# Kernel tuning notes

Hardware: AMD Instinct MI355X
Metric: run time of the kernel (lower is better)

## Reference

```python
import jax, jax.numpy as jnp
import numpy as np

NMUL = 1
NEARZERO = 1e-5
ROUTING_LEN = 15
N_DYN = 3
N_STATIC = 13  # layout includes parRT, parAC (present in STATIC_PARAM_NAMES but unused in the step)


def _descale(x, lb, ub):
    return lb + x * (ub - lb)


def setup_inputs() -> dict:
    key = jax.random.key(0)
    k1, k2, k3 = jax.random.split(key, 3)
    T, G = 365, 50000
    u = jax.random.uniform(k1, (T, G, 3), dtype=jnp.float32)
    prcp = u[..., 0] * 10.0                 # mm/day
    tmean = (u[..., 1] - 0.3) * 20.0        # degC, roughly [-6, 14] so snow branch is exercised
    pet = u[..., 2] * 5.0                   # mm/day
    forcing = jnp.stack([prcp, tmean, pet], axis=-1)
    dyn_raw = jax.random.uniform(k2, (T, G, N_DYN * NMUL), dtype=jnp.float32)
    static_raw = jax.random.uniform(k3, (G, N_STATIC * NMUL + 2), dtype=jnp.float32)
    return {"forcing": forcing, "dyn_raw": dyn_raw, "static_raw": static_raw}


def _hbv_forward(forcing, dyn_raw, static_raw):
    T, G, _ = forcing.shape
    dt = forcing.dtype
    # --- descale dynamic params (per-timestep): parBETA, parK0, parBETAET ---
    dyn = dyn_raw.reshape(T, G, N_DYN, NMUL)
    parBETA = _descale(dyn[:, :, 0], 1.0, 6.0)
    parK0 = _descale(dyn[:, :, 1], 0.05, 0.9)
    parBETAET = _descale(dyn[:, :, 2], 0.3, 5.0)
    # --- descale static params ---
    st = static_raw[:, :N_STATIC * NMUL].reshape(G, N_STATIC, NMUL)
    parFC = _descale(st[:, 0], 50.0, 1000.0)
    parK1 = _descale(st[:, 1], 0.01, 0.5)
    parK2 = _descale(st[:, 2], 0.001, 0.2)
    parLP = _descale(st[:, 3], 0.2, 1.0)
    parPERC = _descale(st[:, 4], 0.0, 10.0)
    parUZL = _descale(st[:, 5], 0.0, 100.0)
    parTT = _descale(st[:, 6], -2.5, 2.5)
    parCFMAX = _descale(st[:, 7], 0.5, 10.0)
    parCFR = _descale(st[:, 8], 0.0, 0.1)
    parCWH = _descale(st[:, 9], 0.0, 0.2)
    parC = _descale(st[:, 10], 0.0, 1.0)
    rout = static_raw[:, N_STATIC * NMUL:]
    rout_a = _descale(rout[:, 0], 0.0, 2.9)
    rout_b = _descale(rout[:, 1], 0.0, 6.5)

    Pm = jnp.broadcast_to(forcing[..., 0:1], (T, G, NMUL))
    Tm = jnp.broadcast_to(forcing[..., 1:2], (T, G, NMUL))
    PETm = jnp.broadcast_to(forcing[..., 2:3], (T, G, NMUL))

    def step(carry, xs):
        SNOWPACK, MELTWATER, SM, SUZ, SLZ = carry
        PRECIP, TEMP, PET, pBETA, pK0, pBETAET = xs
        is_rain = (TEMP >= parTT).astype(dt)
        RAIN = PRECIP * is_rain
        SNOW = PRECIP * (1.0 - is_rain)
        SNOWPACK = SNOWPACK + SNOW
        melt = jnp.minimum(jnp.maximum(parCFMAX * (TEMP - parTT), 0.0), SNOWPACK)
        MELTWATER = MELTWATER + melt
        SNOWPACK = SNOWPACK - melt
        refreezing = jnp.minimum(jnp.maximum(parCFR * parCFMAX * (parTT - TEMP), 0.0), MELTWATER)
        SNOWPACK = SNOWPACK + refreezing
        MELTWATER = MELTWATER - refreezing
        tosoil = jnp.maximum(MELTWATER - parCWH * SNOWPACK, 0.0)
        MELTWATER = MELTWATER - tosoil
        soil_wetness = jnp.clip((SM / parFC) ** pBETA, 0.0, 1.0)
        recharge = (RAIN + tosoil) * soil_wetness
        SM = SM + RAIN + tosoil - recharge
        excess = jnp.maximum(SM - parFC, 0.0)
        SM = SM - excess
        evapfactor = jnp.clip((SM / (parLP * parFC)) ** pBETAET, 0.0, 1.0)
        ETact = jnp.minimum(SM, PET * evapfactor)
        SM = jnp.maximum(SM - ETact, NEARZERO)
        capillary = jnp.minimum(SLZ, parC * SLZ * (1.0 - jnp.minimum(SM / parFC, 1.0)))
        SM = jnp.maximum(SM + capillary, NEARZERO)
        SLZ = jnp.maximum(SLZ - capillary, NEARZERO)
        SUZ = SUZ + recharge + excess
        PERC = jnp.minimum(SUZ, parPERC)
        SUZ = SUZ - PERC
        Q0 = pK0 * jnp.maximum(SUZ - parUZL, 0.0)
        SUZ = SUZ - Q0
        Q1 = parK1 * SUZ
        SUZ = SUZ - Q1
        SLZ = jnp.maximum(SLZ + PERC, 0.0)
        Q2 = parK2 * SLZ
        SLZ = SLZ - Q2
        return (SNOWPACK, MELTWATER, SM, SUZ, SLZ), Q0 + Q1 + Q2

    init = tuple(jnp.full((G, NMUL), 0.001, dtype=dt) for _ in range(5))
    _, Qall = jax.lax.scan(step, init, (Pm, Tm, PETm, parBETA, parK0, parBETAET))
    Qsim = Qall.mean(axis=-1)  # [T, G]: average over nmul components

    # --- gamma unit-hydrograph routing (hydroDL UH_gamma + causal conv, lenF = 15) ---
    aa = jax.nn.relu(rout_a) + 0.1      # shape param, [G]
    theta = jax.nn.relu(rout_b) + 0.5   # scale param, [G]
    t = jnp.arange(0.5, ROUTING_LEN, dtype=dt)[:, None]  # [15, 1] midpoints
    w = (t ** (aa - 1.0)) * jnp.exp(-t / theta) / (jnp.exp(jax.lax.lgamma(aa)) * theta ** aa)
    w = w / w.sum(axis=0)  # [15, G], normalized UH weights
    Qpad = jnp.pad(Qsim, ((ROUTING_LEN - 1, 0), (0, 0)))
    # causal conv: Qrout[t] = sum_k w[k] * Qsim[t-k]; fixed 15-tap loop
    Qrout = sum(w[k] * jax.lax.dynamic_slice_in_dim(Qpad, ROUTING_LEN - 1 - k, T, axis=0)
                for k in range(ROUTING_LEN))
    return Qrout  # streamflow [T, G]


def reference(forcing, dyn_raw, static_raw):
    return _hbv_forward(forcing, dyn_raw, static_raw)
```

## Files before the change

### kernel.cpp

```cpp
#include <hip/hip_runtime.h>

#define NEARZERO 1e-5f
#define RLEN 15
#define LOG2E 1.4426950408889634f

typedef float f32x4 __attribute__((ext_vector_type(4)));
struct __attribute__((packed, aligned(4))) uld4 { f32x4 v; };

static __device__ __forceinline__ f32x4 ld4u(const float* p) {
    return ((const uld4*)p)->v;
}

struct Par { float FC, invFC, invLPFC, K1, K2, PERC, UZL, TT, CFMAX, CFRC, CWH, C; };

#define SB() __builtin_amdgcn_sched_barrier(0)

template<int PH>
__device__ __forceinline__ float one_step(
    float P, float TEMP, float PET, float dx, float dy, float dz,
    const Par& pr,
    float& SNOWPACK, float& MELTWATER, float& SM, float& SUZ, float& SLZ,
    float (&acc)[RLEN], const float (&w)[RLEN])
{
    const float pBETA   = fmaf(dx, 5.0f, 1.0f);
    const float pK0     = fmaf(dy, 0.85f, 0.05f);
    const float pBETAET = fmaf(dz, 4.7f, 0.3f);

    const float d    = TEMP - pr.TT;
    const float RAIN = (d >= 0.0f) ? P : 0.0f;
    const float SNOW = P - RAIN;
    SNOWPACK += SNOW;
    const float melt = __builtin_amdgcn_fmed3f(pr.CFMAX * d, 0.0f, SNOWPACK);
    MELTWATER += melt;
    SNOWPACK  -= melt;
    const float refr = __builtin_amdgcn_fmed3f(pr.CFRC * (0.0f - d), 0.0f, MELTWATER);
    SNOWPACK  += refr;
    MELTWATER -= refr;
    const float tosoil = fmaxf(fmaf(-pr.CWH, SNOWPACK, MELTWATER), 0.0f);
    MELTWATER -= tosoil;

    const float sw = fminf(exp2f(pBETA * __log2f(SM * pr.invFC)), 1.0f);
    const float rt = RAIN + tosoil;
    const float recharge = rt * sw;
    SM = SM + rt - recharge;
    const float excess = fmaxf(SM - pr.FC, 0.0f);
    SM -= excess;
    const float ef = fminf(exp2f(pBETAET * __log2f(SM * pr.invLPFC)), 1.0f);
    const float ETact = fminf(SM, PET * ef);
    SM = fmaxf(SM - ETact, NEARZERO);
    const float capillary = pr.C * SLZ * (1.0f - fminf(SM * pr.invFC, 1.0f));
    SM  = fmaxf(SM + capillary, NEARZERO);
    SLZ = fmaxf(SLZ - capillary, NEARZERO);

    SUZ += recharge + excess;
    const float PERC = fminf(SUZ, pr.PERC);
    SUZ -= PERC;
    const float Q0 = pK0 * fmaxf(SUZ - pr.UZL, 0.0f);
    SUZ -= Q0;
    const float Q1 = pr.K1 * SUZ;
    SUZ -= Q1;
    SLZ += PERC;
    const float Q2 = pr.K2 * SLZ;
    SLZ -= Q2;
    const float Qsim = Q0 + Q1 + Q2;

    const float qr = fmaf(w[0], Qsim, acc[PH]);
    acc[PH] = 0.0f;
#pragma unroll
    for (int k = 1; k < RLEN; ++k) {
        const int j = (PH + k) % RLEN;
        acc[j] = fmaf(w[k], Qsim, acc[j]);
    }
    return qr;
}

template<int PH0>
__device__ __forceinline__ void comp5(
    const f32x4 (&F)[5], const f32x4 (&D)[5], const Par& pr,
    float& SP_, float& MW, float& SM, float& SUZ, float& SLZ,
    float (&acc)[RLEN], const float (&w)[RLEN],
    float*& outp, int G, bool guard)
{
    float qr;
    qr = one_step<(PH0 + 0) % RLEN>(F[0].x, F[0].y, F[0].z, D[0].x, D[0].y, D[0].z,
                                    pr, SP_, MW, SM, SUZ, SLZ, acc, w);
    if (guard) __builtin_nontemporal_store(qr, outp);
    outp += G;
    qr = one_step<(PH0 + 1) % RLEN>(F[1].x, F[1].y, F[1].z, D[1].x, D[1].y, D[1].z,
                                    pr, SP_, MW, SM, SUZ, SLZ, acc, w);
    if (guard) __builtin_nontemporal_store(qr, outp);
    outp += G;
    qr = one_step<(PH0 + 2) % RLEN>(F[2].x, F[2].y, F[2].z, D[2].x, D[2].y, D[2].z,
                                    pr, SP_, MW, SM, SUZ, SLZ, acc, w);
    if (guard) __builtin_nontemporal_store(qr, outp);
    outp += G;
    qr = one_step<(PH0 + 3) % RLEN>(F[3].x, F[3].y, F[3].z, D[3].x, D[3].y, D[3].z,
                                    pr, SP_, MW, SM, SUZ, SLZ, acc, w);
    if (guard) __builtin_nontemporal_store(qr, outp);
    outp += G;
    qr = one_step<(PH0 + 4) % RLEN>(F[4].x, F[4].y, F[4].z, D[4].x, D[4].y, D[4].z,
                                    pr, SP_, MW, SM, SUZ, SLZ, acc, w);
    if (guard) __builtin_nontemporal_store(qr, outp);
    outp += G;
}

__global__ __launch_bounds__(64, 1) void hbv_kernel(
    const float* __restrict__ forcing,
    const float* __restrict__ dynr,
    const float* __restrict__ statr,
    float* __restrict__ out,
    int G)
{
    const int lane = threadIdx.x;
    const int g  = blockIdx.x * 64 + lane;
    const int gc = (g < G) ? g : (G - 1);
    const bool guard = (g < G);

    const float* sp = statr + (size_t)gc * 15;
    Par pr;
    pr.FC    = fmaf(sp[0], 950.0f, 50.0f);
    pr.K1    = fmaf(sp[1], 0.49f, 0.01f);
    pr.K2    = fmaf(sp[2], 0.199f, 0.001f);
    const float parLP = fmaf(sp[3], 0.8f, 0.2f);
    pr.PERC  = sp[4] * 10.0f;
    pr.UZL   = sp[5] * 100.0f;
    pr.TT    = fmaf(sp[6], 5.0f, -2.5f);
    pr.CFMAX = fmaf(sp[7], 9.5f, 0.5f);
    pr.CFRC  = (sp[8] * 0.1f) * pr.CFMAX;
    pr.CWH   = sp[9] * 0.2f;
    pr.C     = sp[10];
    const float rout_a = sp[13] * 2.9f;
    const float rout_b = sp[14] * 6.5f;
    pr.invFC   = 1.0f / pr.FC;
    pr.invLPFC = 1.0f / (parLP * pr.FC);

    const float aa    = fmaxf(rout_a, 0.0f) + 0.1f;
    const float theta = fmaxf(rout_b, 0.0f) + 0.5f;
    const float am1   = aa - 1.0f;
    const float nitl2 = -LOG2E / theta;
    float w[RLEN];
    float wsum = 0.0f;
#pragma unroll
    for (int k = 0; k < RLEN; ++k) {
        const float tk = (float)k + 0.5f;
        w[k] = exp2f(am1 * __log2f(tk) + tk * nitl2);
        wsum += w[k];
    }
    const float winv = 1.0f / wsum;
#pragma unroll
    for (int k = 0; k < RLEN; ++k) w[k] *= winv;

    float SP_ = 0.001f, MW = 0.001f, SM = 0.001f, SUZ = 0.001f, SLZ = 0.001f;
    float acc[RLEN];
#pragma unroll
    for (int k = 0; k < RLEN; ++k) acc[k] = 0.0f;

    const size_t sT = (size_t)G * 3;
    const float* pF = forcing + (size_t)gc * 3;
    const float* pD = dynr    + (size_t)gc * 3;
    float* outp = out + g;

    f32x4 AF[5], AD[5], BF[5], BD[5], CF[5], CD[5];

#define LOADG(BFv, BDv, tb) do { \
    const float* fp_ = pF + (size_t)(tb) * sT; \
    const float* dp_ = pD + (size_t)(tb) * sT; \
    BFv[0] = ld4u(fp_); BDv[0] = ld4u(dp_); fp_ += sT; dp_ += sT; \
    BFv[1] = ld4u(fp_); BDv[1] = ld4u(dp_); fp_ += sT; dp_ += sT; \
    BFv[2] = ld4u(fp_); BDv[2] = ld4u(dp_); fp_ += sT; dp_ += sT; \
    BFv[3] = ld4u(fp_); BDv[3] = ld4u(dp_); fp_ += sT; dp_ += sT; \
    BFv[4] = ld4u(fp_); BDv[4] = ld4u(dp_); \
} while (0)

    LOADG(AF, AD, 0);
    LOADG(BF, BD, 5);

    for (int i = 0; i < 23; ++i) {
        const int tb = i * 15;
        SB(); LOADG(CF, CD, tb + 10); SB();
        comp5<0>(AF, AD, pr, SP_, MW, SM, SUZ, SLZ, acc, w, outp, G, guard);
        SB(); LOADG(AF, AD, tb + 15); SB();
        comp5<5>(BF, BD, pr, SP_, MW, SM, SUZ, SLZ, acc, w, outp, G, guard);
        SB(); LOADG(BF, BD, tb + 20); SB();
        comp5<10>(CF, CD, pr, SP_, MW, SM, SUZ, SLZ, acc, w, outp, G, guard);
    }
    SB(); LOADG(CF, CD, 355); SB();
    comp5<0>(AF, AD, pr, SP_, MW, SM, SUZ, SLZ, acc, w, outp, G, guard);
    SB(); LOADG(AF, AD, 360); SB();
    comp5<5>(BF, BD, pr, SP_, MW, SM, SUZ, SLZ, acc, w, outp, G, guard);
    comp5<10>(CF, CD, pr, SP_, MW, SM, SUZ, SLZ, acc, w, outp, G, guard);
    comp5<0>(AF, AD, pr, SP_, MW, SM, SUZ, SLZ, acc, w, outp, G, guard);
#undef LOADG
}

extern "C" void kernel_launch(void* const* d_in, const int* in_sizes, int n_in,
                              void* d_out, int out_size, void* d_ws, size_t ws_size,
                              hipStream_t stream) {
    const float* forcing = (const float*)d_in[0];
    const float* dynr    = (const float*)d_in[1];
    const float* statr   = (const float*)d_in[2];
    float* out = (float*)d_out;

    const int G = in_sizes[2] / 15;
    const int block = 64;
    const int grid  = (G + block - 1) / block;
    hbv_kernel<<<grid, block, 0, stream>>>(forcing, dynr, statr, out, G);
}
```

Measured before the change: 120.8 us.

## Replace batched register prefetch with per-step loads staged through an LDS ring

Drops the three-buffer, five-step batch prefetch of 16-byte unaligned vector loads. Each timestep now issues 12-byte loads for a row eight steps ahead into a five-slot register set, then moves an earlier register set into a 15-row shared-memory ring that the compute step reads from. The aim is a deeper, evenly spread prefetch pipeline with less register pressure and no over-read past the end of the row. In exchange every step adds LDS writes and reads, and a sched_barrier sits on each step.

```diff
diff --git a/kernel.cpp b/kernel.cpp
--- a/kernel.cpp
+++ b/kernel.cpp
@@ -4,16 +4,13 @@
 #define RLEN 15
 #define LOG2E 1.4426950408889634f
 
-typedef float f32x4 __attribute__((ext_vector_type(4)));
-struct __attribute__((packed, aligned(4))) uld4 { f32x4 v; };
-
-static __device__ __forceinline__ f32x4 ld4u(const float* p) {
-    return ((const uld4*)p)->v;
+struct __attribute__((packed, aligned(4))) F3 { float x, y, z; };
+
+static __device__ __forceinline__ F3 ld3f(const float* p) {
+    return *reinterpret_cast<const F3*>(p);
 }
 
 struct Par { float FC, invFC, invLPFC, K1, K2, PERC, UZL, TT, CFMAX, CFRC, CWH, C; };
-
-#define SB() __builtin_amdgcn_sched_barrier(0)
 
 template<int PH>
 __device__ __forceinline__ float one_step(
@@ -74,36 +71,6 @@
     return qr;
 }
 
-template<int PH0>
-__device__ __forceinline__ void comp5(
-    const f32x4 (&F)[5], const f32x4 (&D)[5], const Par& pr,
-    float& SP_, float& MW, float& SM, float& SUZ, float& SLZ,
-    float (&acc)[RLEN], const float (&w)[RLEN],
-    float*& outp, int G, bool guard)
-{
-    float qr;
-    qr = one_step<(PH0 + 0) % RLEN>(F[0].x, F[0].y, F[0].z, D[0].x, D[0].y, D[0].z,
-                                    pr, SP_, MW, SM, SUZ, SLZ, acc, w);
-    if (guard) __builtin_nontemporal_store(qr, outp);
-    outp += G;
-    qr = one_step<(PH0 + 1) % RLEN>(F[1].x, F[1].y, F[1].z, D[1].x, D[1].y, D[1].z,
-                                    pr, SP_, MW, SM, SUZ, SLZ, acc, w);
-    if (guard) __builtin_nontemporal_store(qr, outp);
-    outp += G;
-    qr = one_step<(PH0 + 2) % RLEN>(F[2].x, F[2].y, F[2].z, D[2].x, D[2].y, D[2].z,
-                                    pr, SP_, MW, SM, SUZ, SLZ, acc, w);
-    if (guard) __builtin_nontemporal_store(qr, outp);
-    outp += G;
-    qr = one_step<(PH0 + 3) % RLEN>(F[3].x, F[3].y, F[3].z, D[3].x, D[3].y, D[3].z,
-                                    pr, SP_, MW, SM, SUZ, SLZ, acc, w);
-    if (guard) __builtin_nontemporal_store(qr, outp);
-    outp += G;
-    qr = one_step<(PH0 + 4) % RLEN>(F[4].x, F[4].y, F[4].z, D[4].x, D[4].y, D[4].z,
-                                    pr, SP_, MW, SM, SUZ, SLZ, acc, w);
-    if (guard) __builtin_nontemporal_store(qr, outp);
-    outp += G;
-}
-
 __global__ __launch_bounds__(64, 1) void hbv_kernel(
     const float* __restrict__ forcing,
     const float* __restrict__ dynr,
@@ -115,6 +82,8 @@
     const int g  = blockIdx.x * 64 + lane;
     const int gc = (g < G) ? g : (G - 1);
     const bool guard = (g < G);
+
+    __shared__ float ring[RLEN][64][6];
 
     const float* sp = statr + (size_t)gc * 15;
     Par pr;
@@ -160,37 +129,79 @@
     const float* pD = dynr    + (size_t)gc * 3;
     float* outp = out + g;
 
-    f32x4 AF[5], AD[5], BF[5], BD[5], CF[5], CD[5];
-
-#define LOADG(BFv, BDv, tb) do { \
-    const float* fp_ = pF + (size_t)(tb) * sT; \
-    const float* dp_ = pD + (size_t)(tb) * sT; \
-    BFv[0] = ld4u(fp_); BDv[0] = ld4u(dp_); fp_ += sT; dp_ += sT; \
-    BFv[1] = ld4u(fp_); BDv[1] = ld4u(dp_); fp_ += sT; dp_ += sT; \
-    BFv[2] = ld4u(fp_); BDv[2] = ld4u(dp_); fp_ += sT; dp_ += sT; \
-    BFv[3] = ld4u(fp_); BDv[3] = ld4u(dp_); fp_ += sT; dp_ += sT; \
-    BFv[4] = ld4u(fp_); BDv[4] = ld4u(dp_); \
+    F3 setF[5], setD[5];
+
+    setF[1] = ld3f(pF + 4 * sT); setD[1] = ld3f(pD + 4 * sT);
+    setF[2] = ld3f(pF + 5 * sT); setD[2] = ld3f(pD + 5 * sT);
+    setF[3] = ld3f(pF + 6 * sT); setD[3] = ld3f(pD + 6 * sT);
+    setF[4] = ld3f(pF + 7 * sT); setD[4] = ld3f(pD + 7 * sT);
+#pragma unroll
+    for (int r = 0; r < 4; ++r) {
+        const F3 f = ld3f(pF + (size_t)r * sT);
+        const F3 d = ld3f(pD + (size_t)r * sT);
+        ring[r][lane][0] = f.x; ring[r][lane][1] = f.y; ring[r][lane][2] = f.z;
+        ring[r][lane][3] = d.x; ring[r][lane][4] = d.y; ring[r][lane][5] = d.z;
+    }
+
+#define STEP(PH, FP, DP) do { \
+    constexpr int P_  = (PH) % RLEN; \
+    constexpr int S_  = P_ % 5; \
+    constexpr int Sw_ = (P_ + 1) % 5; \
+    constexpr int W_  = (P_ + 4) % RLEN; \
+    setF[S_] = ld3f(FP); setD[S_] = ld3f(DP); \
+    __builtin_amdgcn_sched_barrier(0); \
+    const float P2_ = ring[P_][lane][0], T2_ = ring[P_][lane][1], E2_ = ring[P_][lane][2]; \
+    const float x2_ = ring[P_][lane][3], y2_ = ring[P_][lane][4], z2_ = ring[P_][lane][5]; \
+    const float qr_ = one_step<P_>(P2_, T2_, E2_, x2_, y2_, z2_, pr, \
+                                   SP_, MW, SM, SUZ, SLZ, acc, w); \
+    if (guard) __builtin_nontemporal_store(qr_, outp); \
+    outp += G; \
+    ring[W_][lane][0] = setF[Sw_].x; ring[W_][lane][1] = setF[Sw_].y; ring[W_][lane][2] = setF[Sw_].z; \
+    ring[W_][lane][3] = setD[Sw_].x; ring[W_][lane][4] = setD[Sw_].y; ring[W_][lane][5] = setD[Sw_].z; \
 } while (0)
 
-    LOADG(AF, AD, 0);
-    LOADG(BF, BD, 5);
-
+    const float* pFl = pF + 8 * sT;
+    const float* pDl = pD + 8 * sT;
     for (int i = 0; i < 23; ++i) {
-        const int tb = i * 15;
-        SB(); LOADG(CF, CD, tb + 10); SB();
-        comp5<0>(AF, AD, pr, SP_, MW, SM, SUZ, SLZ, acc, w, outp, G, guard);
-        SB(); LOADG(AF, AD, tb + 15); SB();
-        comp5<5>(BF, BD, pr, SP_, MW, SM, SUZ, SLZ, acc, w, outp, G, guard);
-        SB(); LOADG(BF, BD, tb + 20); SB();
-        comp5<10>(CF, CD, pr, SP_, MW, SM, SUZ, SLZ, acc, w, outp, G, guard);
-    }
-    SB(); LOADG(CF, CD, 355); SB();
-    comp5<0>(AF, AD, pr, SP_, MW, SM, SUZ, SLZ, acc, w, outp, G, guard);
-    SB(); LOADG(AF, AD, 360); SB();
-    comp5<5>(BF, BD, pr, SP_, MW, SM, SUZ, SLZ, acc, w, outp, G, guard);
-    comp5<10>(CF, CD, pr, SP_, MW, SM, SUZ, SLZ, acc, w, outp, G, guard);
-    comp5<0>(AF, AD, pr, SP_, MW, SM, SUZ, SLZ, acc, w, outp, G, guard);
-#undef LOADG
+        STEP(0,  pFl, pDl); pFl += sT; pDl += sT;
+        STEP(1,  pFl, pDl); pFl += sT; pDl += sT;
+        STEP(2,  pFl, pDl); pFl += sT; pDl += sT;
+        STEP(3,  pFl, pDl); pFl += sT; pDl += sT;
+        STEP(4,  pFl, pDl); pFl += sT; pDl += sT;
+        STEP(5,  pFl, pDl); pFl += sT; pDl += sT;
+        STEP(6,  pFl, pDl); pFl += sT; pDl += sT;
+        STEP(7,  pFl, pDl); pFl += sT; pDl += sT;
+        STEP(8,  pFl, pDl); pFl += sT; pDl += sT;
+        STEP(9,  pFl, pDl); pFl += sT; pDl += sT;
+        STEP(10, pFl, pDl); pFl += sT; pDl += sT;
+        STEP(11, pFl, pDl); pFl += sT; pDl += sT;
+        STEP(12, pFl, pDl); pFl += sT; pDl += sT;
+        STEP(13, pFl, pDl); pFl += sT; pDl += sT;
+        STEP(14, pFl, pDl); pFl += sT; pDl += sT;
+    }
+#define TROW(T) (((T) + 8 <= 364) ? ((T) + 8) : 364)
+    STEP(0,  pF + (size_t)TROW(345) * sT, pD + (size_t)TROW(345) * sT);
+    STEP(1,  pF + (size_t)TROW(346) * sT, pD + (size_t)TROW(346) * sT);
+    STEP(2,  pF + (size_t)TROW(347) * sT, pD + (size_t)TROW(347) * sT);
+    STEP(3,  pF + (size_t)TROW(348) * sT, pD + (size_t)TROW(348) * sT);
+    STEP(4,  pF + (size_t)TROW(349) * sT, pD + (size_t)TROW(349) * sT);
+    STEP(5,  pF + (size_t)TROW(350) * sT, pD + (size_t)TROW(350) * sT);
+    STEP(6,  pF + (size_t)TROW(351) * sT, pD + (size_t)TROW(351) * sT);
+    STEP(7,  pF + (size_t)TROW(352) * sT, pD + (size_t)TROW(352) * sT);
+    STEP(8,  pF + (size_t)TROW(353) * sT, pD + (size_t)TROW(353) * sT);
+    STEP(9,  pF + (size_t)TROW(354) * sT, pD + (size_t)TROW(354) * sT);
+    STEP(10, pF + (size_t)TROW(355) * sT, pD + (size_t)TROW(355) * sT);
+    STEP(11, pF + (size_t)TROW(356) * sT, pD + (size_t)TROW(356) * sT);
+    STEP(12, pF + (size_t)TROW(357) * sT, pD + (size_t)TROW(357) * sT);
+    STEP(13, pF + (size_t)TROW(358) * sT, pD + (size_t)TROW(358) * sT);
+    STEP(14, pF + (size_t)TROW(359) * sT, pD + (size_t)TROW(359) * sT);
+    STEP(0,  pF + (size_t)TROW(360) * sT, pD + (size_t)TROW(360) * sT);
+    STEP(1,  pF + (size_t)TROW(361) * sT, pD + (size_t)TROW(361) * sT);
+    STEP(2,  pF + (size_t)TROW(362) * sT, pD + (size_t)TROW(362) * sT);
+    STEP(3,  pF + (size_t)TROW(363) * sT, pD + (size_t)TROW(363) * sT);
+    STEP(4,  pF + (size_t)TROW(364) * sT, pD + (size_t)TROW(364) * sT);
+#undef TROW
+#undef STEP
 }
 
 extern "C" void kernel_launch(void* const* d_in, const int* in_sizes, int n_in,
```

New measurement: 111.2 us. 1.09x faster.
